# Optimization experiments

Hardware: AMD Instinct MI355X
Metric: run time of the kernel (lower is better)

## Reference

```python
import jax, jax.numpy as jnp
import numpy as np
from jax import lax

K = 3          # kernel_size
STRIDE = 1
PAD = 1        # (K-1)//2
C = 64         # channels
GC = 16        # group_channels
G = C // GC    # groups = 4
NS = 1         # new_size = ratio * stride
EPS = 1e-5


def mish(x):
    return x * jnp.tanh(jax.nn.softplus(x))


def setup_inputs() -> dict:
    key = jax.random.key(0)
    ks = jax.random.split(key, 4)
    B, H, W = 2, 256, 256
    c1_in = C * K * 2 + G * K * K      # 420
    c1_out = C * NS * NS // 4          # 16
    return {
        "inputs": jax.random.normal(ks[0], (B, C, H, W), jnp.float32),
        "conv1_w": jax.random.normal(ks[1], (c1_out, c1_in, 1, 1), jnp.float32) * 0.05,
        "conv1_b": jnp.zeros((c1_out,), jnp.float32),
        "conv2_w": jax.random.normal(ks[2], (C // 4, C // 4, 3, 3), jnp.float32) * 0.05,
        "conv2_b": jnp.zeros((C // 4,), jnp.float32),
        "conv3_w": jax.random.normal(ks[3], (G * K * K, C // 4, 1, 1), jnp.float32) * 0.05,
        "conv3_b": jnp.zeros((G * K * K,), jnp.float32),
        "bn_gamma": jnp.ones((c1_out,), jnp.float32),
        "bn_beta": jnp.zeros((c1_out,), jnp.float32),
        "bn_mean": jnp.zeros((c1_out,), jnp.float32),
        "bn_var": jnp.ones((c1_out,), jnp.float32),
    }


def _unfold(x, h, w):
    # torch.nn.Unfold(K, 1, PAD, STRIDE): output channel layout (C, kh, kw)
    xp = jnp.pad(x, ((0, 0), (0, 0), (PAD, PAD), (PAD, PAD)))
    cols = [xp[:, :, ki:ki + (h - 1) * STRIDE + 1:STRIDE,
                     kj:kj + (w - 1) * STRIDE + 1:STRIDE]
            for ki in range(K) for kj in range(K)]
    return jnp.stack(cols, axis=2)  # (b, C, K*K, h, w)


def reference(inputs, conv1_w, conv1_b, conv2_w, conv2_b, conv3_w, conv3_b,
              bn_gamma, bn_beta, bn_mean, bn_var):
    b, _, Wd, Hd = inputs.shape
    h = (Wd + 2 * PAD - K) // STRIDE + 1
    w = (Hd + 2 * PAD - K) // STRIDE + 1
    x = _unfold(inputs, h, w).reshape(b, G, GC, K, K, h, w)
    # multi-axis max pooling over (group_channels, kh, kw)
    m_gc = x.max(axis=2).reshape(b, -1, h, w)  # (b, G*K*K, h, w)
    m_kh = x.max(axis=3).reshape(b, -1, h, w)  # (b, C*K, h, w)
    m_kw = x.max(axis=4).reshape(b, -1, h, w)  # (b, C*K, h, w)
    weight = jnp.concatenate([m_gc, m_kh, m_kw], axis=1)  # (b, 420, h, w)
    # conv1 (1x1) + Mish
    weight = mish(jnp.einsum('bihw,oi->bohw', weight, conv1_w[:, :, 0, 0])
                  + conv1_b[None, :, None, None])                  # (b, 16, h, w)
    c = C // 4
    # rearrange 'b (c n1 n2) h w -> (b h w) c n1 n2'
    wn = weight.reshape(b, c, NS, NS, h, w).transpose(0, 4, 5, 1, 2, 3)
    wn = wn.reshape(b * h * w, c, NS, NS)
    wn = lax.conv_general_dilated(wn, conv2_w, (1, 1), ((1, 1), (1, 1)),
                                  dimension_numbers=('NCHW', 'OIHW', 'NCHW'))
    wn = wn + conv2_b[None, :, None, None]
    # rearrange back '(b h w) c n1 n2 -> b (c n1 n2) h w'
    wn = wn.reshape(b, h, w, c, NS, NS).transpose(0, 3, 4, 5, 1, 2)
    wn = wn.reshape(b, c * NS * NS, h, w)
    # BatchNorm (inference form with running stats)
    scale = bn_gamma / jnp.sqrt(bn_var + EPS)
    wn = wn * scale[None, :, None, None] + (bn_beta - bn_mean * scale)[None, :, None, None]
    weight = weight * mish(wn)
    # conv3 (1x1) -> per-pixel attention logits
    weight = jnp.einsum('bihw,oi->bohw', weight, conv3_w[:, :, 0, 0]) \
             + conv3_b[None, :, None, None]                          # (b, G*K*K, h, w)
    weight = jax.nn.softmax(weight.reshape(b, G, 1, K * K, NS * NS, h, w), axis=3)
    # softmax-weighted patch aggregation
    agg = jnp.sum(x.reshape(b, G, GC, K * K, 1, h, w) * weight, axis=3)  # (b,G,GC,NS^2,h,w)
    # fold with kernel=stride=NS (non-overlapping): pure reshape/transpose
    out = agg.reshape(b, C, NS, NS, h, w).transpose(0, 1, 4, 2, 5, 3)
    return out.reshape(b, C, h * NS, w * NS)
```

## Files before the change

### kernel.cpp

```cpp
#include <hip/hip_runtime.h>
#include <math.h>

#define Cch 64
#define Hh  256
#define Ww  256

__device__ __forceinline__ float mishf(float x) {
    float e  = __expf(fminf(x, 15.0f));
    float n  = 1.0f + e;
    float n2 = n * n;
    float t  = __fdividef(n2 - 1.0f, n2 + 1.0f);
    return x > 15.0f ? x : x * t;
}

__global__ __launch_bounds__(256, 8) void revo_kernel(
    const float* __restrict__ in,
    const float* __restrict__ w1, const float* __restrict__ b1,
    const float* __restrict__ w2, const float* __restrict__ b2,
    const float* __restrict__ w3, const float* __restrict__ b3,
    const float* __restrict__ gamma, const float* __restrict__ beta,
    const float* __restrict__ mean,  const float* __restrict__ var,
    float* __restrict__ out)
{
    const int tid  = threadIdx.x;
    const int g    = __builtin_amdgcn_readfirstlane(tid >> 6);
    const int lane = tid & 63;

    const int wseg = blockIdx.x & 3;
    const int h    = (blockIdx.x >> 2) & (Hh - 1);
    const int b    = blockIdx.x >> 10;

    const int w = wseg * 64 + lane;

    __shared__ float lds_y[4][64][17];

    const float* base = in + (size_t)b * Cch * Hh * Ww;

    const bool okm = (w > 0);
    const bool okp = (w < Ww - 1);
    const int offm = okm ? -1 : 0;
    const int offp = okp ?  1 : 0;

    const int hm  = h - 1, hp = h + 1;
    const bool okhm = (hm >= 0), okhp = (hp < Hh);
    const int hmc = okhm ? hm : 0;
    const int hpc = okhp ? hp : Hh - 1;

    float y[16];
    #pragma unroll
    for (int o = 0; o < 16; ++o) y[o] = 0.0f;
    float gmax[9];

    for (int cc = 0; cc < 16; ++cc) {
        const int c = (g << 4) + cc;
        const float* cb = base + (size_t)c * Hh * Ww;
        float p[9];
        {
            const float* rp = cb + (size_t)hmc * Ww + w;
            float v0 = rp[offm], v1 = rp[0], v2 = rp[offp];
            p[0] = (okhm && okm) ? v0 : 0.0f;
            p[1] = okhm ? v1 : 0.0f;
            p[2] = (okhm && okp) ? v2 : 0.0f;
        }
        {
            const float* rp = cb + (size_t)h * Ww + w;
            float v0 = rp[offm], v1 = rp[0], v2 = rp[offp];
            p[3] = okm ? v0 : 0.0f;
            p[4] = v1;
            p[5] = okp ? v2 : 0.0f;
        }
        {
            const float* rp = cb + (size_t)hpc * Ww + w;
            float v0 = rp[offm], v1 = rp[0], v2 = rp[offp];
            p[6] = (okhp && okm) ? v0 : 0.0f;
            p[7] = okhp ? v1 : 0.0f;
            p[8] = (okhp && okp) ? v2 : 0.0f;
        }

        float mkh0 = fmaxf(fmaxf(p[0], p[3]), p[6]);
        float mkh1 = fmaxf(fmaxf(p[1], p[4]), p[7]);
        float mkh2 = fmaxf(fmaxf(p[2], p[5]), p[8]);
        float mkw0 = fmaxf(fmaxf(p[0], p[1]), p[2]);
        float mkw1 = fmaxf(fmaxf(p[3], p[4]), p[5]);
        float mkw2 = fmaxf(fmaxf(p[6], p[7]), p[8]);

        if (cc == 0) {
            #pragma unroll
            for (int k = 0; k < 9; ++k) gmax[k] = p[k];
        } else {
            #pragma unroll
            for (int k = 0; k < 9; ++k) gmax[k] = fmaxf(gmax[k], p[k]);
        }

        #pragma unroll
        for (int o = 0; o < 16; ++o) {
            const float* r = w1 + o * 420;
            y[o] = fmaf(r[ 36 + c * 3 + 0], mkh0, y[o]);
            y[o] = fmaf(r[ 36 + c * 3 + 1], mkh1, y[o]);
            y[o] = fmaf(r[ 36 + c * 3 + 2], mkh2, y[o]);
            y[o] = fmaf(r[228 + c * 3 + 0], mkw0, y[o]);
            y[o] = fmaf(r[228 + c * 3 + 1], mkw1, y[o]);
            y[o] = fmaf(r[228 + c * 3 + 2], mkw2, y[o]);
        }
    }
    #pragma unroll
    for (int o = 0; o < 16; ++o) {
        const float* r = w1 + o * 420 + g * 9;
        #pragma unroll
        for (int k = 0; k < 9; ++k)
            y[o] = fmaf(r[k], gmax[k], y[o]);
    }

    #pragma unroll
    for (int o = 0; o < 16; ++o) lds_y[g][lane][o] = y[o];
    __syncthreads();

    float feat[16];
    #pragma unroll
    for (int o = 0; o < 16; ++o) {
        float t = lds_y[0][lane][o] + lds_y[1][lane][o]
                + lds_y[2][lane][o] + lds_y[3][lane][o] + b1[o];
        feat[o] = mishf(t);
    }

    float feat2[16];
    #pragma unroll
    for (int o = 0; o < 16; ++o) {
        float acc = b2[o];
        #pragma unroll
        for (int i = 0; i < 16; ++i)
            acc = fmaf(w2[o * 144 + i * 9 + 4], feat[i], acc);
        float sc = gamma[o] * rsqrtf(var[o] + 1e-5f);
        acc = acc * sc + (beta[o] - mean[o] * sc);
        feat2[o] = feat[o] * mishf(acc);
    }

    float att[9];
    {
        float mx = -1e30f;
        #pragma unroll
        for (int k = 0; k < 9; ++k) {
            float acc = b3[g * 9 + k];
            #pragma unroll
            for (int i = 0; i < 16; ++i)
                acc = fmaf(w3[(g * 9 + k) * 16 + i], feat2[i], acc);
            att[k] = acc;
            mx = fmaxf(mx, acc);
        }
        float s = 0.0f;
        #pragma unroll
        for (int k = 0; k < 9; ++k) { att[k] = __expf(att[k] - mx); s += att[k]; }
        float inv = __fdividef(1.0f, s);
        #pragma unroll
        for (int k = 0; k < 9; ++k) att[k] *= inv;
    }

    float* ob = out + (((size_t)b * Cch) * Hh + h) * Ww + w;
    for (int gc = 0; gc < 16; ++gc) {
        const int c = (g << 4) + gc;
        const float* cb = base + (size_t)c * Hh * Ww;
        float acc = 0.0f;
        {
            const float* rp = cb + (size_t)hmc * Ww + w;
            float v0 = rp[offm], v1 = rp[0], v2 = rp[offp];
            acc = fmaf((okhm && okm) ? v0 : 0.0f, att[0], acc);
            acc = fmaf(okhm ? v1 : 0.0f,          att[1], acc);
            acc = fmaf((okhm && okp) ? v2 : 0.0f, att[2], acc);
        }
        {
            const float* rp = cb + (size_t)h * Ww + w;
            float v0 = rp[offm], v1 = rp[0], v2 = rp[offp];
            acc = fmaf(okm ? v0 : 0.0f, att[3], acc);
            acc = fmaf(v1,              att[4], acc);
            acc = fmaf(okp ? v2 : 0.0f, att[5], acc);
        }
        {
            const float* rp = cb + (size_t)hpc * Ww + w;
            float v0 = rp[offm], v1 = rp[0], v2 = rp[offp];
            acc = fmaf((okhp && okm) ? v0 : 0.0f, att[6], acc);
            acc = fmaf(okhp ? v1 : 0.0f,          att[7], acc);
            acc = fmaf((okhp && okp) ? v2 : 0.0f, att[8], acc);
        }
        ob[(size_t)c * Hh * Ww] = acc;
    }
}

extern "C" void kernel_launch(void* const* d_in, const int* in_sizes, int n_in,
                              void* d_out, int out_size, void* d_ws, size_t ws_size,
                              hipStream_t stream) {
    const float* in    = (const float*)d_in[0];
    const float* w1    = (const float*)d_in[1];
    const float* b1    = (const float*)d_in[2];
    const float* w2    = (const float*)d_in[3];
    const float* b2    = (const float*)d_in[4];
    const float* w3    = (const float*)d_in[5];
    const float* b3    = (const float*)d_in[6];
    const float* gamma = (const float*)d_in[7];
    const float* beta  = (const float*)d_in[8];
    const float* mean  = (const float*)d_in[9];
    const float* var   = (const float*)d_in[10];
    float* out = (float*)d_out;

    dim3 grid(2 * Hh * 4);
    dim3 block(256);
    hipLaunchKernelGGL(revo_kernel, grid, block, 0, stream,
                       in, w1, b1, w2, b2, w3, b3, gamma, beta, mean, var, out);
}
```

Measured before the change: 92.37 us.

## Prepack conv weights, prefetch next channel loads, and remap block order

Adds a single-block prep kernel that repacks conv1/conv2 weights into contiguous per-channel layouts and folds the batchnorm scale and offset, so the main kernel reads weights sequentially. Software-pipelines the per-channel 3x3 neighbourhood loads by prefetching the next channel into registers, in both the reduction and the aggregation loops. Remaps block IDs so consecutive blocks are spread across rows, and relaxes launch bounds from 8 to 4 waves per SIMD. The extra launch and the higher register pressure from the double buffer could offset the gains.

```diff
diff --git a/kernel.cpp b/kernel.cpp
--- a/kernel.cpp
+++ b/kernel.cpp
@@ -4,6 +4,13 @@
 #define Cch 64
 #define Hh  256
 #define Ww  256
+
+#define WS_WPA   0
+#define WS_WGC   6144
+#define WS_WC2   6720
+#define WS_SC    6976
+#define WS_OFF   6992
+#define WS_FLOATS 7008
 
 __device__ __forceinline__ float mishf(float x) {
     float e  = __expf(fminf(x, 15.0f));
@@ -13,22 +20,51 @@
     return x > 15.0f ? x : x * t;
 }
 
-__global__ __launch_bounds__(256, 8) void revo_kernel(
-    const float* __restrict__ in,
-    const float* __restrict__ w1, const float* __restrict__ b1,
-    const float* __restrict__ w2, const float* __restrict__ b2,
-    const float* __restrict__ w3, const float* __restrict__ b3,
+__global__ __launch_bounds__(256) void prep_kernel(
+    const float* __restrict__ w1, const float* __restrict__ w2,
+    const float* __restrict__ b2,
     const float* __restrict__ gamma, const float* __restrict__ beta,
     const float* __restrict__ mean,  const float* __restrict__ var,
+    float* __restrict__ ws)
+{
+    for (int idx = threadIdx.x; idx < 6144; idx += 256) {
+        int c = idx / 96, r = idx % 96, o = r / 6, j = r % 6;
+        float v = (j < 3) ? w1[o * 420 + 36 + c * 3 + j]
+                          : w1[o * 420 + 228 + c * 3 + (j - 3)];
+        ws[WS_WPA + idx] = v;
+    }
+    for (int idx = threadIdx.x; idx < 576; idx += 256) {
+        int g = idx / 144, rem = idx % 144, o = rem / 9, k = rem % 9;
+        ws[WS_WGC + idx] = w1[o * 420 + g * 9 + k];
+    }
+    for (int idx = threadIdx.x; idx < 256; idx += 256) {
+        int o = idx / 16, i = idx % 16;
+        ws[WS_WC2 + idx] = w2[o * 144 + i * 9 + 4];
+    }
+    if (threadIdx.x < 16) {
+        int o = threadIdx.x;
+        float sc = gamma[o] * rsqrtf(var[o] + 1e-5f);
+        ws[WS_SC + o]  = sc;
+        ws[WS_OFF + o] = b2[o] * sc + beta[o] - mean[o] * sc;
+    }
+}
+
+__global__ __launch_bounds__(256, 4) void revo_kernel(
+    const float* __restrict__ in,
+    const float* __restrict__ b1,
+    const float* __restrict__ w3, const float* __restrict__ b3,
+    const float* __restrict__ ws,
     float* __restrict__ out)
 {
     const int tid  = threadIdx.x;
     const int g    = __builtin_amdgcn_readfirstlane(tid >> 6);
     const int lane = tid & 63;
 
-    const int wseg = blockIdx.x & 3;
-    const int h    = (blockIdx.x >> 2) & (Hh - 1);
-    const int b    = blockIdx.x >> 10;
+    const int bid     = blockIdx.x;
+    const int logical = ((bid & 7) << 8) + (bid >> 3);
+    const int wseg = logical & 3;
+    const int h    = (logical >> 2) & (Hh - 1);
+    const int b    = logical >> 10;
 
     const int w = wseg * 64 + lane;
 
@@ -41,7 +77,7 @@
     const int offm = okm ? -1 : 0;
     const int offp = okp ?  1 : 0;
 
-    const int hm  = h - 1, hp = h + 1;
+    const int hm = h - 1, hp = h + 1;
     const bool okhm = (hm >= 0), okhp = (hp < Hh);
     const int hmc = okhm ? hm : 0;
     const int hpc = okhp ? hp : Hh - 1;
@@ -51,64 +87,77 @@
     for (int o = 0; o < 16; ++o) y[o] = 0.0f;
     float gmax[9];
 
+    const float* wpA = ws + WS_WPA + (size_t)(g << 4) * 96;
+
+    float p[9], pn[9];
+    {
+        const float* cb = base + (size_t)(g << 4) * Hh * Ww;
+        const float* r0 = cb + (size_t)hmc * Ww + w;
+        const float* r1 = cb + (size_t)h   * Ww + w;
+        const float* r2 = cb + (size_t)hpc * Ww + w;
+        p[0] = r0[offm]; p[1] = r0[0]; p[2] = r0[offp];
+        p[3] = r1[offm]; p[4] = r1[0]; p[5] = r1[offp];
+        p[6] = r2[offm]; p[7] = r2[0]; p[8] = r2[offp];
+    }
+
     for (int cc = 0; cc < 16; ++cc) {
-        const int c = (g << 4) + cc;
-        const float* cb = base + (size_t)c * Hh * Ww;
-        float p[9];
-        {
-            const float* rp = cb + (size_t)hmc * Ww + w;
-            float v0 = rp[offm], v1 = rp[0], v2 = rp[offp];
-            p[0] = (okhm && okm) ? v0 : 0.0f;
-            p[1] = okhm ? v1 : 0.0f;
-            p[2] = (okhm && okp) ? v2 : 0.0f;
-        }
-        {
-            const float* rp = cb + (size_t)h * Ww + w;
-            float v0 = rp[offm], v1 = rp[0], v2 = rp[offp];
-            p[3] = okm ? v0 : 0.0f;
-            p[4] = v1;
-            p[5] = okp ? v2 : 0.0f;
-        }
-        {
-            const float* rp = cb + (size_t)hpc * Ww + w;
-            float v0 = rp[offm], v1 = rp[0], v2 = rp[offp];
-            p[6] = (okhp && okm) ? v0 : 0.0f;
-            p[7] = okhp ? v1 : 0.0f;
-            p[8] = (okhp && okp) ? v2 : 0.0f;
-        }
-
-        float mkh0 = fmaxf(fmaxf(p[0], p[3]), p[6]);
-        float mkh1 = fmaxf(fmaxf(p[1], p[4]), p[7]);
-        float mkh2 = fmaxf(fmaxf(p[2], p[5]), p[8]);
-        float mkw0 = fmaxf(fmaxf(p[0], p[1]), p[2]);
-        float mkw1 = fmaxf(fmaxf(p[3], p[4]), p[5]);
-        float mkw2 = fmaxf(fmaxf(p[6], p[7]), p[8]);
+        if (cc < 15) {
+            const float* cb = base + (size_t)((g << 4) + cc + 1) * Hh * Ww;
+            const float* r0 = cb + (size_t)hmc * Ww + w;
+            const float* r1 = cb + (size_t)h   * Ww + w;
+            const float* r2 = cb + (size_t)hpc * Ww + w;
+            pn[0] = r0[offm]; pn[1] = r0[0]; pn[2] = r0[offp];
+            pn[3] = r1[offm]; pn[4] = r1[0]; pn[5] = r1[offp];
+            pn[6] = r2[offm]; pn[7] = r2[0]; pn[8] = r2[offp];
+        }
+
+        float q[9];
+        q[0] = (okhm && okm) ? p[0] : 0.0f;
+        q[1] =  okhm         ? p[1] : 0.0f;
+        q[2] = (okhm && okp) ? p[2] : 0.0f;
+        q[3] =  okm          ? p[3] : 0.0f;
+        q[4] =  p[4];
+        q[5] =  okp          ? p[5] : 0.0f;
+        q[6] = (okhp && okm) ? p[6] : 0.0f;
+        q[7] =  okhp         ? p[7] : 0.0f;
+        q[8] = (okhp && okp) ? p[8] : 0.0f;
+
+        float mkh0 = fmaxf(fmaxf(q[0], q[3]), q[6]);
+        float mkh1 = fmaxf(fmaxf(q[1], q[4]), q[7]);
+        float mkh2 = fmaxf(fmaxf(q[2], q[5]), q[8]);
+        float mkw0 = fmaxf(fmaxf(q[0], q[1]), q[2]);
+        float mkw1 = fmaxf(fmaxf(q[3], q[4]), q[5]);
+        float mkw2 = fmaxf(fmaxf(q[6], q[7]), q[8]);
 
         if (cc == 0) {
             #pragma unroll
-            for (int k = 0; k < 9; ++k) gmax[k] = p[k];
+            for (int k = 0; k < 9; ++k) gmax[k] = q[k];
         } else {
             #pragma unroll
-            for (int k = 0; k < 9; ++k) gmax[k] = fmaxf(gmax[k], p[k]);
-        }
-
+            for (int k = 0; k < 9; ++k) gmax[k] = fmaxf(gmax[k], q[k]);
+        }
+
+        const float* r = wpA + cc * 96;
         #pragma unroll
         for (int o = 0; o < 16; ++o) {
-            const float* r = w1 + o * 420;
-            y[o] = fmaf(r[ 36 + c * 3 + 0], mkh0, y[o]);
-            y[o] = fmaf(r[ 36 + c * 3 + 1], mkh1, y[o]);
-            y[o] = fmaf(r[ 36 + c * 3 + 2], mkh2, y[o]);
-            y[o] = fmaf(r[228 + c * 3 + 0], mkw0, y[o]);
-            y[o] = fmaf(r[228 + c * 3 + 1], mkw1, y[o]);
-            y[o] = fmaf(r[228 + c * 3 + 2], mkw2, y[o]);
-        }
-    }
-    #pragma unroll
-    for (int o = 0; o < 16; ++o) {
-        const float* r = w1 + o * 420 + g * 9;
-        #pragma unroll
-        for (int k = 0; k < 9; ++k)
-            y[o] = fmaf(r[k], gmax[k], y[o]);
+            y[o] = fmaf(r[o * 6 + 0], mkh0, y[o]);
+            y[o] = fmaf(r[o * 6 + 1], mkh1, y[o]);
+            y[o] = fmaf(r[o * 6 + 2], mkh2, y[o]);
+            y[o] = fmaf(r[o * 6 + 3], mkw0, y[o]);
+            y[o] = fmaf(r[o * 6 + 4], mkw1, y[o]);
+            y[o] = fmaf(r[o * 6 + 5], mkw2, y[o]);
+        }
+
+        #pragma unroll
+        for (int k = 0; k < 9; ++k) p[k] = pn[k];
+    }
+    {
+        const float* r = ws + WS_WGC + g * 144;
+        #pragma unroll
+        for (int o = 0; o < 16; ++o)
+            #pragma unroll
+            for (int k = 0; k < 9; ++k)
+                y[o] = fmaf(r[o * 9 + k], gmax[k], y[o]);
     }
 
     #pragma unroll
@@ -124,15 +173,18 @@
     }
 
     float feat2[16];
-    #pragma unroll
-    for (int o = 0; o < 16; ++o) {
-        float acc = b2[o];
-        #pragma unroll
-        for (int i = 0; i < 16; ++i)
-            acc = fmaf(w2[o * 144 + i * 9 + 4], feat[i], acc);
-        float sc = gamma[o] * rsqrtf(var[o] + 1e-5f);
-        acc = acc * sc + (beta[o] - mean[o] * sc);
-        feat2[o] = feat[o] * mishf(acc);
+    {
+        const float* wc2 = ws + WS_WC2;
+        const float* sc  = ws + WS_SC;
+        const float* off = ws + WS_OFF;
+        #pragma unroll
+        for (int o = 0; o < 16; ++o) {
+            float acc = 0.0f;
+            #pragma unroll
+            for (int i = 0; i < 16; ++i)
+                acc = fmaf(wc2[o * 16 + i], feat[i], acc);
+            feat2[o] = feat[o] * mishf(acc * sc[o] + off[o]);
+        }
     }
 
     float att[9];
@@ -141,9 +193,10 @@
         #pragma unroll
         for (int k = 0; k < 9; ++k) {
             float acc = b3[g * 9 + k];
+            const float* r = w3 + (g * 9 + k) * 16;
             #pragma unroll
             for (int i = 0; i < 16; ++i)
-                acc = fmaf(w3[(g * 9 + k) * 16 + i], feat2[i], acc);
+                acc = fmaf(r[i], feat2[i], acc);
             att[k] = acc;
             mx = fmaxf(mx, acc);
         }
@@ -156,32 +209,39 @@
     }
 
     float* ob = out + (((size_t)b * Cch) * Hh + h) * Ww + w;
+    {
+        const float* cb = base + (size_t)(g << 4) * Hh * Ww;
+        const float* r0 = cb + (size_t)hmc * Ww + w;
+        const float* r1 = cb + (size_t)h   * Ww + w;
+        const float* r2 = cb + (size_t)hpc * Ww + w;
+        p[0] = r0[offm]; p[1] = r0[0]; p[2] = r0[offp];
+        p[3] = r1[offm]; p[4] = r1[0]; p[5] = r1[offp];
+        p[6] = r2[offm]; p[7] = r2[0]; p[8] = r2[offp];
+    }
     for (int gc = 0; gc < 16; ++gc) {
-        const int c = (g << 4) + gc;
-        const float* cb = base + (size_t)c * Hh * Ww;
+        if (gc < 15) {
+            const float* cb = base + (size_t)((g << 4) + gc + 1) * Hh * Ww;
+            const float* r0 = cb + (size_t)hmc * Ww + w;
+            const float* r1 = cb + (size_t)h   * Ww + w;
+            const float* r2 = cb + (size_t)hpc * Ww + w;
+            pn[0] = r0[offm]; pn[1] = r0[0]; pn[2] = r0[offp];
+            pn[3] = r1[offm]; pn[4] = r1[0]; pn[5] = r1[offp];
+            pn[6] = r2[offm]; pn[7] = r2[0]; pn[8] = r2[offp];
+        }
         float acc = 0.0f;
-        {
-            const float* rp = cb + (size_t)hmc * Ww + w;
-            float v0 = rp[offm], v1 = rp[0], v2 = rp[offp];
-            acc = fmaf((okhm && okm) ? v0 : 0.0f, att[0], acc);
-            acc = fmaf(okhm ? v1 : 0.0f,          att[1], acc);
-            acc = fmaf((okhm && okp) ? v2 : 0.0f, att[2], acc);
-        }
-        {
-            const float* rp = cb + (size_t)h * Ww + w;
-            float v0 = rp[offm], v1 = rp[0], v2 = rp[offp];
-            acc = fmaf(okm ? v0 : 0.0f, att[3], acc);
-            acc = fmaf(v1,              att[4], acc);
-            acc = fmaf(okp ? v2 : 0.0f, att[5], acc);
-        }
-        {
-            const float* rp = cb + (size_t)hpc * Ww + w;
-            float v0 = rp[offm], v1 = rp[0], v2 = rp[offp];
-            acc = fmaf((okhp && okm) ? v0 : 0.0f, att[6], acc);
-            acc = fmaf(okhp ? v1 : 0.0f,          att[7], acc);
-            acc = fmaf((okhp && okp) ? v2 : 0.0f, att[8], acc);
-        }
-        ob[(size_t)c * Hh * Ww] = acc;
+        acc = fmaf((okhm && okm) ? p[0] : 0.0f, att[0], acc);
+        acc = fmaf( okhm         ? p[1] : 0.0f, att[1], acc);
+        acc = fmaf((okhm && okp) ? p[2] : 0.0f, att[2], acc);
+        acc = fmaf( okm          ? p[3] : 0.0f, att[3], acc);
+        acc = fmaf( p[4],                       att[4], acc);
+        acc = fmaf( okp          ? p[5] : 0.0f, att[5], acc);
+        acc = fmaf((okhp && okm) ? p[6] : 0.0f, att[6], acc);
+        acc = fmaf( okhp         ? p[7] : 0.0f, att[7], acc);
+        acc = fmaf((okhp && okp) ? p[8] : 0.0f, att[8], acc);
+        ob[(size_t)((g << 4) + gc) * Hh * Ww] = acc;
+
+        #pragma unroll
+        for (int k = 0; k < 9; ++k) p[k] = pn[k];
     }
 }
 
@@ -200,9 +260,13 @@
     const float* mean  = (const float*)d_in[9];
     const float* var   = (const float*)d_in[10];
     float* out = (float*)d_out;
+    float* ws  = (float*)d_ws;
+
+    hipLaunchKernelGGL(prep_kernel, dim3(1), dim3(256), 0, stream,
+                       w1, w2, b2, gamma, beta, mean, var, ws);
 
     dim3 grid(2 * Hh * 4);
     dim3 block(256);
     hipLaunchKernelGGL(revo_kernel, grid, block, 0, stream,
-                       in, w1, b1, w2, b2, w3, b3, gamma, beta, mean, var, out);
-}
+                       in, b1, w3, b3, ws, out);
+}
```

Measured after the change: 97.96 us. 6.0% more time.
